# Kernel tuning notes

Measured on AMD Instinct MI355X. Metric: run time of the kernel, lower is better.

Reference implementation:

```python
import jax, jax.numpy as jnp
import numpy as np

N_IMAGE, N_REGIONS = 128, 36
N_CAPTION, N_WORD = 128, 32
D = 1024
LAMBDA_SOFTMAX = 20.0
EPS = 1e-8
LEAKY_SLOPE = 0.1


def setup_inputs() -> dict:
    key = jax.random.key(0)
    k1, k2 = jax.random.split(key)
    images = jax.random.normal(k1, (N_IMAGE, N_REGIONS, D), dtype=jnp.float32)
    captions = jax.random.normal(k2, (N_CAPTION, N_WORD, D), dtype=jnp.float32)
    # all captions at max length so the per-caption loop vectorizes exactly
    cap_lens = jnp.full((N_CAPTION,), N_WORD, dtype=jnp.int32)
    return {"images": images, "captions": captions, "cap_lens": cap_lens}


def _l2norm(x, axis):
    return x / (jnp.linalg.norm(x, axis=axis, keepdims=True) + EPS)


def _focal_attn(raw):
    # raw: (..., S, Q) = context @ query^T, as in torch bmm(context, queryT)
    a = jax.nn.leaky_relu(raw, LEAKY_SLOPE)
    a = _l2norm(a, axis=-1)              # l2norm over queryL (dim=2 in torch)
    a = jnp.swapaxes(a, -1, -2)          # (..., Q, S)
    a = jax.nn.softmax(a * LAMBDA_SOFTMAX, axis=-1)
    # focal_equal: funcF = attn*S - sum_j attn_j ; mask where positive
    S = a.shape[-1]
    funcF = a * S - jnp.sum(a, axis=-1, keepdims=True)
    fattn = jnp.where(funcF > 0, 1.0, 0.0).astype(a.dtype)
    tmp = fattn * a
    return tmp / jnp.sum(tmp, axis=-1, keepdims=True)  # renormalized attn (..., Q, S)


def _cosine(a, b):
    # torch F.cosine_similarity semantics along last axis
    na = jnp.maximum(jnp.linalg.norm(a, axis=-1), EPS)
    nb = jnp.maximum(jnp.linalg.norm(b, axis=-1), EPS)
    return jnp.sum(a * b, axis=-1) / (na * nb)


def reference(images, captions, cap_lens):
    # images: (I, R, d); captions: (C, W, d); all cap_lens == W (vectorized loop)
    # ---- t2i: query = caption words, context = image regions ----
    raw_t2i = jnp.einsum('ird,cwd->cirw', images, captions)   # (C, I, R=S, W=Q)
    re_t2i = _focal_attn(raw_t2i)                             # (C, I, W, R)
    wctx_t2i = jnp.einsum('ciwr,ird->ciwd', re_t2i, images)   # (C, I, W, d)
    t2i = _cosine(captions[:, None, :, :], wctx_t2i).mean(axis=-1)  # (C, I)
    # ---- i2t: query = image regions, context = caption words ----
    raw_i2t = jnp.einsum('cwd,ird->ciwr', captions, images)   # (C, I, W=S, R=Q)
    re_i2t = _focal_attn(raw_i2t)                             # (C, I, R, W)
    wctx_i2t = jnp.einsum('cirw,cwd->cird', re_i2t, captions) # (C, I, R, d)
    i2t = _cosine(images[None, :, :, :], wctx_i2t).mean(axis=-1)    # (C, I)
    return (t2i + i2t).T                                      # (n_image, n_caption)
```

## Files before the change

kernel.cpp:

```cpp
#include <hip/hip_runtime.h>
#include <math.h>

#define NR 36
#define NW 32
#define DD 1024
#define EPSF 1e-8f

typedef _Float16 f16x8 __attribute__((ext_vector_type(8)));
typedef float f32x16 __attribute__((ext_vector_type(16)));
#define MFMA32(a, b, c) __builtin_amdgcn_mfma_f32_32x32x16_f16((a), (b), (c), 0, 0, 0)
#define GLD16(srcp, dstp)                                                              \
  __builtin_amdgcn_global_load_lds((const __attribute__((address_space(1))) void*)(srcp), \
                                   (__attribute__((address_space(3))) void*)(dstp), 16, 0, 0)

__device__ __forceinline__ float leakyf(float x) { return x > 0.f ? x : 0.1f * x; }

__global__ __launch_bounds__(256) void prep_kernel(
    const float* __restrict__ img, const float* __restrict__ cap,
    float* __restrict__ Gimg, float* __restrict__ Gcap,
    float* __restrict__ imgn, float* __restrict__ capn,
    _Float16* __restrict__ Ahf, _Float16* __restrict__ Alf,
    _Float16* __restrict__ Bhf, _Float16* __restrict__ Blf) {
  __shared__ float sA[2][NR][64];
  const int t = threadIdx.x;
  if (blockIdx.x < 128) {
    const int i = blockIdx.x;
    const float* A = img + (size_t)i * NR * DD;
    int ti = 0, tj = 0;
    const bool active = t < 171;
    if (active) {
      int rem = t, rl = 18;
      while (rem >= rl) { rem -= rl; ++ti; --rl; }
      tj = ti + rem;
    }
    const int a0 = 2 * ti, a1 = 2 * ti + 1, b0 = 2 * tj, b1 = 2 * tj + 1;
    const int sza = ti & 7, szb = tj & 7;
    const int kq8_1 = t / NR, r1 = t - kq8_1 * NR;
    const bool has2 = t < 32;
    const int s2 = t + 256;
    const int kq8_2 = s2 / NR, r2 = s2 - kq8_2 * NR;
    float4 p0a, p1a, p0b, p1b;
    float g00 = 0.f, g01 = 0.f, g10 = 0.f, g11 = 0.f;

    auto loadRegs = [&](int idx) {
      const int k0 = idx * 64;
      p0a = *(const float4*)(A + r1 * DD + k0 + kq8_1 * 8);
      p1a = *(const float4*)(A + r1 * DD + k0 + kq8_1 * 8 + 4);
      if (has2) {
        p0b = *(const float4*)(A + r2 * DD + k0 + kq8_2 * 8);
        p1b = *(const float4*)(A + r2 * DD + k0 + kq8_2 * 8 + 4);
      }
    };
    auto cw = [&](int idx, int cur) {
      const int k0 = idx * 64;
      {
        const float a[8] = {p0a.x, p0a.y, p0a.z, p0a.w, p1a.x, p1a.y, p1a.z, p1a.w};
        f16x8 hv;
#pragma unroll
        for (int j = 0; j < 8; ++j) hv[j] = (_Float16)a[j];
        const int m = i * NR + r1, mt = m >> 5, ml = m & 31;
        const int kk = k0 + kq8_1 * 8;
        const size_t fo = (((size_t)mt * 128 + (kk >> 3)) * 32 + ml) * 8;
        *(f16x8*)(Ahf + fo) = hv;
        const int sw = (r1 >> 1) & 7;
        *(float4*)&sA[cur][r1][((2 * kq8_1) ^ sw) * 4] = p0a;
        *(float4*)&sA[cur][r1][((2 * kq8_1 + 1) ^ sw) * 4] = p1a;
      }
      if (has2) {
        const float a[8] = {p0b.x, p0b.y, p0b.z, p0b.w, p1b.x, p1b.y, p1b.z, p1b.w};
        f16x8 hv;
#pragma unroll
        for (int j = 0; j < 8; ++j) hv[j] = (_Float16)a[j];
        const int m = i * NR + r2, mt = m >> 5, ml = m & 31;
        const int kk = k0 + kq8_2 * 8;
        const size_t fo = (((size_t)mt * 128 + (kk >> 3)) * 32 + ml) * 8;
        *(f16x8*)(Ahf + fo) = hv;
        const int sw = (r2 >> 1) & 7;
        *(float4*)&sA[cur][r2][((2 * kq8_2) ^ sw) * 4] = p0b;
        *(float4*)&sA[cur][r2][((2 * kq8_2 + 1) ^ sw) * 4] = p1b;
      }
    };

    loadRegs(0);
    for (int idx = 0; idx < 16; ++idx) {
      const int cur = idx & 1;
      cw(idx, cur);
      if (idx < 15) loadRegs(idx + 1);
      __syncthreads();
      if (active) {
#pragma unroll
        for (int k = 0; k < 16; ++k) {
          const float4 va0 = *(const float4*)&sA[cur][a0][(k ^ sza) * 4];
          const float4 va1 = *(const float4*)&sA[cur][a1][(k ^ sza) * 4];
          const float4 vb0 = *(const float4*)&sA[cur][b0][(k ^ szb) * 4];
          const float4 vb1 = *(const float4*)&sA[cur][b1][(k ^ szb) * 4];
          g00 = fmaf(va0.x, vb0.x, g00); g00 = fmaf(va0.y, vb0.y, g00);
          g00 = fmaf(va0.z, vb0.z, g00); g00 = fmaf(va0.w, vb0.w, g00);
          g01 = fmaf(va0.x, vb1.x, g01); g01 = fmaf(va0.y, vb1.y, g01);
          g01 = fmaf(va0.z, vb1.z, g01); g01 = fmaf(va0.w, vb1.w, g01);
          g10 = fmaf(va1.x, vb0.x, g10); g10 = fmaf(va1.y, vb0.y, g10);
          g10 = fmaf(va1.z, vb0.z, g10); g10 = fmaf(va1.w, vb0.w, g10);
          g11 = fmaf(va1.x, vb1.x, g11); g11 = fmaf(va1.y, vb1.y, g11);
          g11 = fmaf(va1.z, vb1.z, g11); g11 = fmaf(va1.w, vb1.w, g11);
        }
      }
    }
    if (active) {
      float* Gi = Gimg + (size_t)i * NR * NR;
      Gi[a0 * NR + b0] = g00; Gi[b0 * NR + a0] = g00;
      Gi[a0 * NR + b1] = g01; Gi[b1 * NR + a0] = g01;
      Gi[a1 * NR + b0] = g10; Gi[b0 * NR + a1] = g10;
      Gi[a1 * NR + b1] = g11; Gi[b1 * NR + a1] = g11;
      if (ti == tj) {
        imgn[i * NR + a0] = fmaxf(sqrtf(g00), EPSF);
        imgn[i * NR + a1] = fmaxf(sqrtf(g11), EPSF);
      }
    }
  } else {
    const int cb = blockIdx.x - 128;
    const float* A = cap + (size_t)cb * NW * DD;
    int ti = 0, tj = 0;
    const bool active = t < 136;
    if (active) {
      int rem = t, rl = 16;
      while (rem >= rl) { rem -= rl; ++ti; --rl; }
      tj = ti + rem;
    }
    const int a0 = 2 * ti, a1 = 2 * ti + 1, b0 = 2 * tj, b1 = 2 * tj + 1;
    const int sza = ti & 7, szb = tj & 7;
    const int kq8_1 = t >> 5, r1 = t & 31;
    float4 p0a, p1a;
    float g00 = 0.f, g01 = 0.f, g10 = 0.f, g11 = 0.f;

    auto loadRegs = [&](int idx) {
      const int k0 = idx * 64;
      p0a = *(const float4*)(A + r1 * DD + k0 + kq8_1 * 8);
      p1a = *(const float4*)(A + r1 * DD + k0 + kq8_1 * 8 + 4);
    };
    auto cw = [&](int idx, int cur) {
      const int k0 = idx * 64;
      const float a[8] = {p0a.x, p0a.y, p0a.z, p0a.w, p1a.x, p1a.y, p1a.z, p1a.w};
      f16x8 hv;
#pragma unroll
      for (int j = 0; j < 8; ++j) hv[j] = (_Float16)a[j];
      const int kk = k0 + kq8_1 * 8;
      const size_t fo = (((size_t)cb * 128 + (kk >> 3)) * 32 + r1) * 8;
      *(f16x8*)(Bhf + fo) = hv;
      const int sw = (r1 >> 1) & 7;
      *(float4*)&sA[cur][r1][((2 * kq8_1) ^ sw) * 4] = p0a;
      *(float4*)&sA[cur][r1][((2 * kq8_1 + 1) ^ sw) * 4] = p1a;
    };

    loadRegs(0);
    for (int idx = 0; idx < 16; ++idx) {
      const int cur = idx & 1;
      cw(idx, cur);
      if (idx < 15) loadRegs(idx + 1);
      __syncthreads();
      if (active) {
#pragma unroll
        for (int k = 0; k < 16; ++k) {
          const float4 va0 = *(const float4*)&sA[cur][a0][(k ^ sza) * 4];
          const float4 va1 = *(const float4*)&sA[cur][a1][(k ^ sza) * 4];
          const float4 vb0 = *(const float4*)&sA[cur][b0][(k ^ szb) * 4];
          const float4 vb1 = *(const float4*)&sA[cur][b1][(k ^ szb) * 4];
          g00 = fmaf(va0.x, vb0.x, g00); g00 = fmaf(va0.y, vb0.y, g00);
          g00 = fmaf(va0.z, vb0.z, g00); g00 = fmaf(va0.w, vb0.w, g00);
          g01 = fmaf(va0.x, vb1.x, g01); g01 = fmaf(va0.y, vb1.y, g01);
          g01 = fmaf(va0.z, vb1.z, g01); g01 = fmaf(va0.w, vb1.w, g01);
          g10 = fmaf(va1.x, vb0.x, g10); g10 = fmaf(va1.y, vb0.y, g10);
          g10 = fmaf(va1.z, vb0.z, g10); g10 = fmaf(va1.w, vb0.w, g10);
          g11 = fmaf(va1.x, vb1.x, g11); g11 = fmaf(va1.y, vb1.y, g11);
          g11 = fmaf(va1.z, vb1.z, g11); g11 = fmaf(va1.w, vb1.w, g11);
        }
      }
    }
    if (active) {
      float* Gc = Gcap + (size_t)cb * NW * NW;
      Gc[a0 * NW + b0] = g00; Gc[b0 * NW + a0] = g00;
      Gc[a0 * NW + b1] = g01; Gc[b1 * NW + a0] = g01;
      Gc[a1 * NW + b0] = g10; Gc[b0 * NW + a1] = g10;
      Gc[a1 * NW + b1] = g11; Gc[b1 * NW + a1] = g11;
      if (ti == tj) {
        capn[cb * NW + a0] = fmaxf(sqrtf(g00), EPSF);
        capn[cb * NW + a1] = fmaxf(sqrtf(g11), EPSF);
      }
    }
  }
}

__device__ __forceinline__ void gemm_loadA(const _Float16* __restrict__ Ahf, int Mt0, int kt,
                                           int kb, int lm, f16x8 ar[2][2]) {
#pragma unroll
  for (int mt = 0; mt < 2; ++mt)
#pragma unroll
    for (int ks = 0; ks < 2; ++ks) {
      const size_t o = (((size_t)(Mt0 + mt) * 128) + kt * 4 + ks * 2 + kb) * 256 + lm * 8;
      ar[mt][ks] = *(const f16x8*)(Ahf + o);
    }
}

__global__ __launch_bounds__(256) void mfma_gemm_kernel(
    const _Float16* __restrict__ Ahf, const _Float16* __restrict__ Alf,
    const _Float16* __restrict__ Bhf, const _Float16* __restrict__ Blf, float* __restrict__ C) {
  __shared__ _Float16 sB[2][8192];
  const int bid0 = blockIdx.x;
  const int bid = (bid0 & 7) * 144 + (bid0 >> 3);
  const int yb = bid & 31, xb = bid >> 5;
  const int n0b = yb * 4;
  const int tid = threadIdx.x;
  const int wv = tid >> 6, lane = tid & 63;
  const int lm = lane & 31, kb = lane >> 5;
  const int Mt0 = xb * 4 + (wv >> 1) * 2;
  const int nb0 = (wv & 1) * 2;
  (void)Alf; (void)Blf;

  auto stageB2 = [&](int p, int buf) {
#pragma unroll
    for (int u = 0; u < 4; ++u) {
      const int kt = 2 * p + (u >> 1);
      const int cpb = wv * 4 + (u & 1) * 2;
      const int cp = cpb + kb;
      const int nb = cp >> 2, kq = cp & 3;
      const _Float16* src = Bhf + (((size_t)(n0b + nb) * 128 + kt * 4 + kq) * 32 + lm) * 8;
      GLD16(src, &sB[buf][(u >> 1) * 4096 + cpb * 256]);
    }
  };

  f32x16 acc[2][2];
#pragma unroll
  for (int a = 0; a < 2; ++a)
#pragma unroll
    for (int b = 0; b < 2; ++b) acc[a][b] = {};
  f16x8 arE[2][2][2], arO[2][2][2];

  auto loadA2 = [&](int p, f16x8 ar[2][2][2]) {
#pragma unroll
    for (int kh = 0; kh < 2; ++kh) gemm_loadA(Ahf, Mt0, 2 * p + kh, kb, lm, ar[kh]);
  };
  auto computeHalf = [&](const _Float16* sb, const f16x8 ar[2][2]) {
#pragma unroll
    for (int ks = 0; ks < 2; ++ks)
#pragma unroll
      for (int ntl = 0; ntl < 2; ++ntl) {
        const int nt = nb0 + ntl;
        const int co = (nt * 4 + ks * 2 + kb) * 256 + lm * 8;
        const f16x8 bh = *(const f16x8*)&sb[co];
        acc[0][ntl] = MFMA32(ar[0][ks], bh, acc[0][ntl]);
        acc[1][ntl] = MFMA32(ar[1][ks], bh, acc[1][ntl]);
      }
  };
  auto computeP = [&](const _Float16* sb, const f16x8 ar[2][2][2]) {
    computeHalf(sb, ar[0]);
    computeHalf(sb + 4096, ar[1]);
  };

  stageB2(0, 0);
  loadA2(0, arE);
  for (int pp = 0; pp < 8; ++pp) {
    const int p = 2 * pp;
    __syncthreads();
    stageB2(p + 1, 1);
    loadA2(p + 1, arO);
    computeP(sB[0], arE);
    __syncthreads();
    if (p + 2 < 16) {
      stageB2(p + 2, 0);
      loadA2(p + 2, arE);
    }
    computeP(sB[1], arO);
  }
#pragma unroll
  for (int mt = 0; mt < 2; ++mt)
#pragma unroll
    for (int ntl = 0; ntl < 2; ++ntl) {
      const int cc = n0b + nb0 + ntl;
      const f32x16 a = acc[mt][ntl];
#pragma unroll
      for (int q = 0; q < 16; ++q) {
        const int row32 = (q & 3) + 8 * (q >> 2) + 4 * kb;
        const int m = (Mt0 + mt) * 32 + row32;
        const int il = m / NR, r = m - il * NR;
        C[((size_t)il * 128 + cc) * (NR * NW) + r * NW + lm] = a[q];
      }
    }
}

#define GCP 1040
__global__ __launch_bounds__(192, 4) void fused_attn_kernel(
    const float* __restrict__ C, const float* __restrict__ Gimg, const float* __restrict__ Gcap,
    const float* __restrict__ imgn, const float* __restrict__ capn, float* __restrict__ out) {
  const int i = blockIdx.x;
  const int cg = blockIdx.y;
  const int tid = threadIdx.x;
  const int wv = tid >> 6, lane = tid & 63;
  __shared__ float sS[2][NR * 36];
  __shared__ float sGi[NR * NR];
  __shared__ float sGc[2 * GCP];
  __shared__ float sInvR[2][NR];
  __shared__ float sInvC[2][NW];
  __shared__ float sVal[72];
  __shared__ float red[2];
  if (tid < 2) red[tid] = 0.f;
  const float* Cp = C + ((size_t)i * 128 + cg * 2) * (NR * NW);
  for (int t = tid; t < 2 * 288; t += 192) {
    const int cap = t / 288, rem = t - cap * 288;
    const int r = rem >> 3, wq = rem & 7;
    const float4 v = *(const float4*)(Cp + cap * (NR * NW) + r * NW + wq * 4);
    *(float4*)&sS[cap][r * 36 + wq * 4] = v;
  }
  const float* Gi = Gimg + (size_t)i * (NR * NR);
  for (int t = tid; t < 324; t += 192) *(float4*)&sGi[t * 4] = *(const float4*)(Gi + t * 4);
  const float* Gc0 = Gcap + (size_t)(cg * 2) * (NW * NW);
  for (int t = tid; t < 512; t += 192) {
    const int cap = t >> 8, q = t & 255;
    *(float4*)&sGc[cap * GCP + q * 4] = *(const float4*)(Gc0 + cap * (NW * NW) + q * 4);
  }
  __syncthreads();
  if (tid < 64) {
    const int cap = tid >> 5, w = tid & 31;
    float c0 = 0.f, c1 = 0.f, c2 = 0.f, c3 = 0.f;
#pragma unroll
    for (int j = 0; j < NR; j += 4) {
      const float l0 = leakyf(sS[cap][(j + 0) * 36 + w]);
      const float l1 = leakyf(sS[cap][(j + 1) * 36 + w]);
      const float l2 = leakyf(sS[cap][(j + 2) * 36 + w]);
      const float l3 = leakyf(sS[cap][(j + 3) * 36 + w]);
      c0 = fmaf(l0, l0, c0); c1 = fmaf(l1, l1, c1);
      c2 = fmaf(l2, l2, c2); c3 = fmaf(l3, l3, c3);
    }
    sInvC[cap][w] = 20.f / (sqrtf((c0 + c1) + (c2 + c3)) + EPSF);
  } else if (tid < 136) {
    const int u = tid - 64;
    const int cap = u / NR, r = u - cap * NR;
    float r0 = 0.f, r1 = 0.f, r2 = 0.f, r3 = 0.f;
#pragma unroll
    for (int k = 0; k < 8; ++k) {
      const float4 v = *(const float4*)&sS[cap][r * 36 + k * 4];
      float l;
      l = leakyf(v.x); r0 = fmaf(l, l, r0);
      l = leakyf(v.y); r1 = fmaf(l, l, r1);
      l = leakyf(v.z); r2 = fmaf(l, l, r2);
      l = leakyf(v.w); r3 = fmaf(l, l, r3);
    }
    sInvR[cap][r] = 20.f / (sqrtf((r0 + r1) + (r2 + r3)) + EPSF);
  }
  __syncthreads();
  if (tid < 64) {
    const int cap = tid >> 5, w = tid & 31;
    float z[NR];
    float m0 = -1e30f, m1 = -1e30f, m2 = -1e30f, m3 = -1e30f;
#pragma unroll
    for (int j = 0; j < NR; j += 4) {
      z[j + 0] = leakyf(sS[cap][(j + 0) * 36 + w]) * sInvR[cap][j + 0]; m0 = fmaxf(m0, z[j + 0]);
      z[j + 1] = leakyf(sS[cap][(j + 1) * 36 + w]) * sInvR[cap][j + 1]; m1 = fmaxf(m1, z[j + 1]);
      z[j + 2] = leakyf(sS[cap][(j + 2) * 36 + w]) * sInvR[cap][j + 2]; m2 = fmaxf(m2, z[j + 2]);
      z[j + 3] = leakyf(sS[cap][(j + 3) * 36 + w]) * sInvR[cap][j + 3]; m3 = fmaxf(m3, z[j + 3]);
    }
    const float mz = fmaxf(fmaxf(m0, m1), fmaxf(m2, m3));
    float a0 = 0.f, a1 = 0.f, a2 = 0.f, a3 = 0.f;
#pragma unroll
    for (int j = 0; j < NR; j += 4) {
      z[j + 0] = __expf(z[j + 0] - mz); a0 += z[j + 0];
      z[j + 1] = __expf(z[j + 1] - mz); a1 += z[j + 1];
      z[j + 2] = __expf(z[j + 2] - mz); a2 += z[j + 2];
      z[j + 3] = __expf(z[j + 3] - mz); a3 += z[j + 3];
    }
    const float thr = ((a0 + a1) + (a2 + a3)) * (1.f / NR);
    float n0 = 0.f, n1 = 0.f, n2 = 0.f, n3 = 0.f;
#pragma unroll
    for (int j = 0; j < NR; j += 4) {
      z[j + 0] = (z[j + 0] > thr) ? z[j + 0] : 0.f;
      n0 = fmaf(z[j + 0], sS[cap][(j + 0) * 36 + w], n0);
      z[j + 1] = (z[j + 1] > thr) ? z[j + 1] : 0.f;
      n1 = fmaf(z[j + 1], sS[cap][(j + 1) * 36 + w], n1);
      z[j + 2] = (z[j + 2] > thr) ? z[j + 2] : 0.f;
      n2 = fmaf(z[j + 2], sS[cap][(j + 2) * 36 + w], n2);
      z[j + 3] = (z[j + 3] > thr) ? z[j + 3] : 0.f;
      n3 = fmaf(z[j + 3], sS[cap][(j + 3) * 36 + w], n3);
    }
    const float num = (n0 + n1) + (n2 + n3);
    float d0 = 0.f, d1 = 0.f, d2 = 0.f, d3 = 0.f;
#pragma unroll
    for (int j = 0; j < NR; ++j) {
      const int cj = j >> 2;
      float h0, h1, h2, h3;
      {
        const float4 g = *(const float4*)&sGi[j * 36 + cj * 4];
        const float ge[4] = {g.x, g.y, g.z, g.w};
        h0 = 0.5f * ge[j & 3] * z[j];
        h1 = 0.f; h2 = 0.f; h3 = 0.f;
#pragma unroll
        for (int e = 0; e < 4; ++e) {
          const int k = cj * 4 + e;
          if (k > j) h1 = fmaf(ge[e], z[k], h1);
        }
      }
#pragma unroll
      for (int c = 0; c < 9; ++c) {
        if (c > cj) {
          const float4 g = *(const float4*)&sGi[j * 36 + c * 4];
          h0 = fmaf(g.x, z[c * 4 + 0], h0);
          h1 = fmaf(g.y, z[c * 4 + 1], h1);
          h2 = fmaf(g.z, z[c * 4 + 2], h2);
          h3 = fmaf(g.w, z[c * 4 + 3], h3);
        }
      }
      const float h = (h0 + h1) + (h2 + h3);
      if ((j & 3) == 0) d0 = fmaf(z[j], h, d0);
      else if ((j & 3) == 1) d1 = fmaf(z[j], h, d1);
      else if ((j & 3) == 2) d2 = fmaf(z[j], h, d2);
      else d3 = fmaf(z[j], h, d3);
    }
    const float den2 = (d0 + d1) + (d2 + d3);
    const float val = num / (capn[(cg * 2 + cap) * NW + w] * sqrtf(2.f * den2) + 1e-30f);
    float contrib = val * (1.f / NW);
#pragma unroll
    for (int d = 1; d < 32; d <<= 1) contrib += __shfl_xor(contrib, d, 64);
    if ((tid & 31) == 0) atomicAdd(&red[cap], contrib);
  } else if (lane < 36) {
    const int u = (wv - 1) * 36 + lane;
    const int cap = u / NR, r = u - cap * NR;
    float z[NW];
    float m0 = -1e30f, m1 = -1e30f, m2 = -1e30f, m3 = -1e30f;
#pragma unroll
    for (int k = 0; k < 8; ++k) {
      const float4 v = *(const float4*)&sS[cap][r * 36 + k * 4];
      z[k * 4 + 0] = leakyf(v.x) * sInvC[cap][k * 4 + 0]; m0 = fmaxf(m0, z[k * 4 + 0]);
      z[k * 4 + 1] = leakyf(v.y) * sInvC[cap][k * 4 + 1]; m1 = fmaxf(m1, z[k * 4 + 1]);
      z[k * 4 + 2] = leakyf(v.z) * sInvC[cap][k * 4 + 2]; m2 = fmaxf(m2, z[k * 4 + 2]);
      z[k * 4 + 3] = leakyf(v.w) * sInvC[cap][k * 4 + 3]; m3 = fmaxf(m3, z[k * 4 + 3]);
    }
    const float mz = fmaxf(fmaxf(m0, m1), fmaxf(m2, m3));
    float a0 = 0.f, a1 = 0.f, a2 = 0.f, a3 = 0.f;
#pragma unroll
    for (int w = 0; w < NW; w += 4) {
      z[w + 0] = __expf(z[w + 0] - mz); a0 += z[w + 0];
      z[w + 1] = __expf(z[w + 1] - mz); a1 += z[w + 1];
      z[w + 2] = __expf(z[w + 2] - mz); a2 += z[w + 2];
      z[w + 3] = __expf(z[w + 3] - mz); a3 += z[w + 3];
    }
    const float thr = ((a0 + a1) + (a2 + a3)) * (1.f / NW);
    float n0 = 0.f, n1 = 0.f, n2 = 0.f, n3 = 0.f;
#pragma unroll
    for (int k = 0; k < 8; ++k) {
      const float4 v = *(const float4*)&sS[cap][r * 36 + k * 4];
      z[k * 4 + 0] = (z[k * 4 + 0] > thr) ? z[k * 4 + 0] : 0.f;
      n0 = fmaf(z[k * 4 + 0], v.x, n0);
      z[k * 4 + 1] = (z[k * 4 + 1] > thr) ? z[k * 4 + 1] : 0.f;
      n1 = fmaf(z[k * 4 + 1], v.y, n1);
      z[k * 4 + 2] = (z[k * 4 + 2] > thr) ? z[k * 4 + 2] : 0.f;
      n2 = fmaf(z[k * 4 + 2], v.z, n2);
      z[k * 4 + 3] = (z[k * 4 + 3] > thr) ? z[k * 4 + 3] : 0.f;
      n3 = fmaf(z[k * 4 + 3], v.w, n3);
    }
    const float num = (n0 + n1) + (n2 + n3);
    const float* Gp = &sGc[cap * GCP];
    float d0 = 0.f, d1 = 0.f, d2 = 0.f, d3 = 0.f;
#pragma unroll
    for (int w = 0; w < NW; ++w) {
      const int cw = w >> 2;
      float h0, h1, h2, h3;
      {
        const float4 g = *(const float4*)&Gp[w * 32 + cw * 4];
        const float ge[4] = {g.x, g.y, g.z, g.w};
        h0 = 0.5f * ge[w & 3] * z[w];
        h1 = 0.f; h2 = 0.f; h3 = 0.f;
#pragma unroll
        for (int e = 0; e < 4; ++e) {
          const int k = cw * 4 + e;
          if (k > w) h1 = fmaf(ge[e], z[k], h1);
        }
      }
#pragma unroll
      for (int c = 0; c < 8; ++c) {
        if (c > cw) {
          const float4 g = *(const float4*)&Gp[w * 32 + c * 4];
          h0 = fmaf(g.x, z[c * 4 + 0], h0);
          h1 = fmaf(g.y, z[c * 4 + 1], h1);
          h2 = fmaf(g.z, z[c * 4 + 2], h2);
          h3 = fmaf(g.w, z[c * 4 + 3], h3);
        }
      }
      const float h = (h0 + h1) + (h2 + h3);
      if ((w & 3) == 0) d0 = fmaf(z[w], h, d0);
      else if ((w & 3) == 1) d1 = fmaf(z[w], h, d1);
      else if ((w & 3) == 2) d2 = fmaf(z[w], h, d2);
      else d3 = fmaf(z[w], h, d3);
    }
    const float den2 = (d0 + d1) + (d2 + d3);
    const float val = num / (imgn[i * NR + r] * sqrtf(2.f * den2) + 1e-30f);
    sVal[u] = val * (1.f / NR);
  }
  __syncthreads();
  if (tid < 64) {
    const int cap = tid >> 5, x = tid & 31;
    float v = sVal[cap * 36 + x];
    if (x < 4) v += sVal[cap * 36 + 32 + x];
#pragma unroll
    for (int d = 1; d < 32; d <<= 1) v += __shfl_xor(v, d, 64);
    if ((tid & 31) == 0) atomicAdd(&red[cap], v);
  }
  __syncthreads();
  if (tid < 2) out[(size_t)i * 128 + cg * 2 + tid] = red[tid];
}

extern "C" void kernel_launch(void* const* d_in, const int* in_sizes, int n_in,
                              void* d_out, int out_size, void* d_ws, size_t ws_size,
                              hipStream_t stream) {
  (void)in_sizes; (void)n_in; (void)out_size; (void)ws_size;
  const float* images = (const float*)d_in[0];
  const float* captions = (const float*)d_in[1];
  float* out = (float*)d_out;

  char* wb = (char*)d_ws;
  _Float16* Ahf = (_Float16*)wb; wb += (size_t)4608 * 1024 * 2;
  _Float16* Alf = (_Float16*)wb; wb += (size_t)4608 * 1024 * 2;
  _Float16* Bhf = (_Float16*)wb; wb += (size_t)4096 * 1024 * 2;
  _Float16* Blf = (_Float16*)wb; wb += (size_t)4096 * 1024 * 2;
  float* Gimg = (float*)wb; wb += (size_t)128 * NR * NR * 4;
  float* Gcap = (float*)wb; wb += (size_t)128 * NW * NW * 4;
  float* imgn = (float*)wb; wb += (size_t)128 * NR * 4;
  float* capn = (float*)wb; wb += (size_t)128 * NW * 4;
  float* C = (float*)wb;

  prep_kernel<<<256, 256, 0, stream>>>(images, captions, Gimg, Gcap, imgn, capn,
                                       Ahf, Alf, Bhf, Blf);
  mfma_gemm_kernel<<<1152, 256, 0, stream>>>(Ahf, Alf, Bhf, Blf, C);
  fused_attn_kernel<<<dim3(128, 64), 192, 0, stream>>>(C, Gimg, Gcap, imgn, capn, out);
}
```

Measured before the change: 235.6 us.

## Split prep Gram computation over K into four slabs, reduce in attention kernel

The prep kernel now launches four blocks per image/caption, each handling a quarter of the D dimension and writing a partial Gram matrix to its own slab. The attention kernel sums the four partial slabs when loading the Gram matrices into shared memory and derives the row norms from the Gram diagonal instead of separate norm buffers. This aims to raise parallelism in the prep stage, which had only 256 blocks doing long serial loops. In exchange it adds extra global reads in the attention kernel and a second barrier per iteration. Unused Alf/Blf workspace pointers are also removed.

```diff
diff --git a/kernel.cpp b/kernel.cpp
--- a/kernel.cpp
+++ b/kernel.cpp
@@ -15,16 +15,18 @@
 
 __device__ __forceinline__ float leakyf(float x) { return x > 0.f ? x : 0.1f * x; }
 
+#define GI_SLAB (128 * NR * NR)
+#define GC_SLAB (128 * NW * NW)
+
 __global__ __launch_bounds__(256) void prep_kernel(
     const float* __restrict__ img, const float* __restrict__ cap,
     float* __restrict__ Gimg, float* __restrict__ Gcap,
-    float* __restrict__ imgn, float* __restrict__ capn,
-    _Float16* __restrict__ Ahf, _Float16* __restrict__ Alf,
-    _Float16* __restrict__ Bhf, _Float16* __restrict__ Blf) {
+    _Float16* __restrict__ Ahf, _Float16* __restrict__ Bhf) {
   __shared__ float sA[2][NR][64];
   const int t = threadIdx.x;
-  if (blockIdx.x < 128) {
-    const int i = blockIdx.x;
+  const int x = blockIdx.x;
+  if (x < 512) {
+    const int i = x >> 2, kh = x & 3;
     const float* A = img + (size_t)i * NR * DD;
     int ti = 0, tj = 0;
     const bool active = t < 171;
@@ -81,11 +83,13 @@
       }
     };
 
-    loadRegs(0);
-    for (int idx = 0; idx < 16; ++idx) {
-      const int cur = idx & 1;
+    const int idx0 = kh * 4;
+    loadRegs(idx0);
+    for (int l = 0; l < 4; ++l) {
+      const int idx = idx0 + l;
+      const int cur = l & 1;
       cw(idx, cur);
-      if (idx < 15) loadRegs(idx + 1);
+      if (l < 3) loadRegs(idx + 1);
       __syncthreads();
       if (active) {
 #pragma unroll
@@ -104,20 +108,18 @@
           g11 = fmaf(va1.z, vb1.z, g11); g11 = fmaf(va1.w, vb1.w, g11);
         }
       }
+      __syncthreads();
     }
     if (active) {
-      float* Gi = Gimg + (size_t)i * NR * NR;
+      float* Gi = Gimg + (size_t)kh * GI_SLAB + (size_t)i * NR * NR;
       Gi[a0 * NR + b0] = g00; Gi[b0 * NR + a0] = g00;
       Gi[a0 * NR + b1] = g01; Gi[b1 * NR + a0] = g01;
       Gi[a1 * NR + b0] = g10; Gi[b0 * NR + a1] = g10;
       Gi[a1 * NR + b1] = g11; Gi[b1 * NR + a1] = g11;
-      if (ti == tj) {
-        imgn[i * NR + a0] = fmaxf(sqrtf(g00), EPSF);
-        imgn[i * NR + a1] = fmaxf(sqrtf(g11), EPSF);
-      }
     }
   } else {
-    const int cb = blockIdx.x - 128;
+    const int xc = x - 512;
+    const int cb = xc >> 2, kh = xc & 3;
     const float* A = cap + (size_t)cb * NW * DD;
     int ti = 0, tj = 0;
     const bool active = t < 136;
@@ -151,11 +153,13 @@
       *(float4*)&sA[cur][r1][((2 * kq8_1 + 1) ^ sw) * 4] = p1a;
     };
 
-    loadRegs(0);
-    for (int idx = 0; idx < 16; ++idx) {
-      const int cur = idx & 1;
+    const int idx0 = kh * 4;
+    loadRegs(idx0);
+    for (int l = 0; l < 4; ++l) {
+      const int idx = idx0 + l;
+      const int cur = l & 1;
       cw(idx, cur);
-      if (idx < 15) loadRegs(idx + 1);
+      if (l < 3) loadRegs(idx + 1);
       __syncthreads();
       if (active) {
 #pragma unroll
@@ -174,17 +178,14 @@
           g11 = fmaf(va1.z, vb1.z, g11); g11 = fmaf(va1.w, vb1.w, g11);
         }
       }
+      __syncthreads();
     }
     if (active) {
-      float* Gc = Gcap + (size_t)cb * NW * NW;
+      float* Gc = Gcap + (size_t)kh * GC_SLAB + (size_t)cb * NW * NW;
       Gc[a0 * NW + b0] = g00; Gc[b0 * NW + a0] = g00;
       Gc[a0 * NW + b1] = g01; Gc[b1 * NW + a0] = g01;
       Gc[a1 * NW + b0] = g10; Gc[b0 * NW + a1] = g10;
       Gc[a1 * NW + b1] = g11; Gc[b1 * NW + a1] = g11;
-      if (ti == tj) {
-        capn[cb * NW + a0] = fmaxf(sqrtf(g00), EPSF);
-        capn[cb * NW + a1] = fmaxf(sqrtf(g11), EPSF);
-      }
     }
   }
 }
@@ -201,8 +202,7 @@
 }
 
 __global__ __launch_bounds__(256) void mfma_gemm_kernel(
-    const _Float16* __restrict__ Ahf, const _Float16* __restrict__ Alf,
-    const _Float16* __restrict__ Bhf, const _Float16* __restrict__ Blf, float* __restrict__ C) {
+    const _Float16* __restrict__ Ahf, const _Float16* __restrict__ Bhf, float* __restrict__ C) {
   __shared__ _Float16 sB[2][8192];
   const int bid0 = blockIdx.x;
   const int bid = (bid0 & 7) * 144 + (bid0 >> 3);
@@ -213,7 +213,6 @@
   const int lm = lane & 31, kb = lane >> 5;
   const int Mt0 = xb * 4 + (wv >> 1) * 2;
   const int nb0 = (wv & 1) * 2;
-  (void)Alf; (void)Blf;
 
   auto stageB2 = [&](int p, int buf) {
 #pragma unroll
@@ -289,7 +288,7 @@
 #define GCP 1040
 __global__ __launch_bounds__(192, 4) void fused_attn_kernel(
     const float* __restrict__ C, const float* __restrict__ Gimg, const float* __restrict__ Gcap,
-    const float* __restrict__ imgn, const float* __restrict__ capn, float* __restrict__ out) {
+    float* __restrict__ out) {
   const int i = blockIdx.x;
   const int cg = blockIdx.y;
   const int tid = threadIdx.x;
@@ -310,11 +309,31 @@
     *(float4*)&sS[cap][r * 36 + wq * 4] = v;
   }
   const float* Gi = Gimg + (size_t)i * (NR * NR);
-  for (int t = tid; t < 324; t += 192) *(float4*)&sGi[t * 4] = *(const float4*)(Gi + t * 4);
+  for (int t = tid; t < 324; t += 192) {
+    const float4 g0 = *(const float4*)(Gi + t * 4);
+    const float4 g1 = *(const float4*)(Gi + GI_SLAB + t * 4);
+    const float4 g2 = *(const float4*)(Gi + 2 * GI_SLAB + t * 4);
+    const float4 g3 = *(const float4*)(Gi + 3 * GI_SLAB + t * 4);
+    float4 s;
+    s.x = (g0.x + g1.x) + (g2.x + g3.x);
+    s.y = (g0.y + g1.y) + (g2.y + g3.y);
+    s.z = (g0.z + g1.z) + (g2.z + g3.z);
+    s.w = (g0.w + g1.w) + (g2.w + g3.w);
+    *(float4*)&sGi[t * 4] = s;
+  }
   const float* Gc0 = Gcap + (size_t)(cg * 2) * (NW * NW);
   for (int t = tid; t < 512; t += 192) {
     const int cap = t >> 8, q = t & 255;
-    *(float4*)&sGc[cap * GCP + q * 4] = *(const float4*)(Gc0 + cap * (NW * NW) + q * 4);
+    const float4 g0 = *(const float4*)(Gc0 + cap * (NW * NW) + q * 4);
+    const float4 g1 = *(const float4*)(Gc0 + GC_SLAB + cap * (NW * NW) + q * 4);
+    const float4 g2 = *(const float4*)(Gc0 + 2 * GC_SLAB + cap * (NW * NW) + q * 4);
+    const float4 g3 = *(const float4*)(Gc0 + 3 * GC_SLAB + cap * (NW * NW) + q * 4);
+    float4 s;
+    s.x = (g0.x + g1.x) + (g2.x + g3.x);
+    s.y = (g0.y + g1.y) + (g2.y + g3.y);
+    s.z = (g0.z + g1.z) + (g2.z + g3.z);
+    s.w = (g0.w + g1.w) + (g2.w + g3.w);
+    *(float4*)&sGc[cap * GCP + q * 4] = s;
   }
   __syncthreads();
   if (tid < 64) {
@@ -413,7 +432,8 @@
       else d3 = fmaf(z[j], h, d3);
     }
     const float den2 = (d0 + d1) + (d2 + d3);
-    const float val = num / (capn[(cg * 2 + cap) * NW + w] * sqrtf(2.f * den2) + 1e-30f);
+    const float cn = fmaxf(sqrtf(sGc[cap * GCP + w * 33]), EPSF);
+    const float val = num / (cn * sqrtf(2.f * den2) + 1e-30f);
     float contrib = val * (1.f / NW);
 #pragma unroll
     for (int d = 1; d < 32; d <<= 1) contrib += __shfl_xor(contrib, d, 64);
@@ -489,7 +509,8 @@
       else d3 = fmaf(z[w], h, d3);
     }
     const float den2 = (d0 + d1) + (d2 + d3);
-    const float val = num / (imgn[i * NR + r] * sqrtf(2.f * den2) + 1e-30f);
+    const float rn = fmaxf(sqrtf(sGi[r * 37]), EPSF);
+    const float val = num / (rn * sqrtf(2.f * den2) + 1e-30f);
     sVal[u] = val * (1.f / NR);
   }
   __syncthreads();
@@ -515,17 +536,12 @@
 
   char* wb = (char*)d_ws;
   _Float16* Ahf = (_Float16*)wb; wb += (size_t)4608 * 1024 * 2;
-  _Float16* Alf = (_Float16*)wb; wb += (size_t)4608 * 1024 * 2;
   _Float16* Bhf = (_Float16*)wb; wb += (size_t)4096 * 1024 * 2;
-  _Float16* Blf = (_Float16*)wb; wb += (size_t)4096 * 1024 * 2;
-  float* Gimg = (float*)wb; wb += (size_t)128 * NR * NR * 4;
-  float* Gcap = (float*)wb; wb += (size_t)128 * NW * NW * 4;
-  float* imgn = (float*)wb; wb += (size_t)128 * NR * 4;
-  float* capn = (float*)wb; wb += (size_t)128 * NW * 4;
+  float* Gimg = (float*)wb; wb += (size_t)4 * GI_SLAB * 4;
+  float* Gcap = (float*)wb; wb += (size_t)4 * GC_SLAB * 4;
   float* C = (float*)wb;
 
-  prep_kernel<<<256, 256, 0, stream>>>(images, captions, Gimg, Gcap, imgn, capn,
-                                       Ahf, Alf, Bhf, Blf);
-  mfma_gemm_kernel<<<1152, 256, 0, stream>>>(Ahf, Alf, Bhf, Blf, C);
-  fused_attn_kernel<<<dim3(128, 64), 192, 0, stream>>>(C, Gimg, Gcap, imgn, capn, out);
+  prep_kernel<<<1024, 256, 0, stream>>>(images, captions, Gimg, Gcap, Ahf, Bhf);
+  mfma_gemm_kernel<<<1152, 256, 0, stream>>>(Ahf, Bhf, C);
+  fused_attn_kernel<<<dim3(128, 64), 192, 0, stream>>>(C, Gimg, Gcap, out);
 }
```

Measured after the change: 229.7 us, median of 2. -2.5%, faster.
